# Kernel tuning notes

Hardware: AMD Instinct MI355X
Metric: run time of the kernel (lower is better)

The kernel has to match this reference:

```python
import jax, jax.numpy as jnp
import numpy as np

N, DIN, DOUT, R, H = 3072, 128, 128, 3, 4


def setup_inputs() -> dict:
    key = jax.random.key(0)
    k0, k1, k2, k3 = jax.random.split(key, 4)
    features = jax.random.normal(k0, (N, DIN), jnp.float32)
    adjacency = jax.random.randint(k1, (R, N, N), 0, 2, jnp.int32)
    W = jax.random.normal(k2, (R, DOUT, DIN), jnp.float32) * (1.0 / np.sqrt(DIN))  # Linear weights (out,in)
    hd = DOUT // H
    a = jax.random.normal(k3, (R, 2 * hd), jnp.float32) * (1.0 / np.sqrt(2 * hd))  # attention vectors
    bias = jnp.zeros((DOUT,), jnp.float32)
    return {"features": features, "adjacency": adjacency, "W": W, "a": a,
            "bias": bias, "num_heads": H}


def reference(features, adjacency, W, a, bias, num_heads):
    # features: [N, Din], adjacency: [R, N, N] int, W: [R, Dout, Din],
    # a: [R, 2*head_dim], bias: [Dout]
    Rr, Dout = W.shape[0], W.shape[1]
    Nn = features.shape[0]
    hd = Dout // num_heads
    # per-relation linear transform -> [R, N, H, hd]
    t = jnp.einsum('nd,rod->rno', features, W).reshape(Rr, Nn, num_heads, hd)
    # additive attention: score(i,j,h) = a_src . t[i,h] + a_dst . t[j,h]
    s_src = jnp.einsum('rnhd,rd->rnh', t, a[:, :hd])
    s_dst = jnp.einsum('rnhd,rd->rnh', t, a[:, hd:])
    mask = (adjacency != 0)[..., None]  # [R, N, N, 1]
    # original fills NON-edges with 0 (not -inf), then softmaxes over j incl. zeros
    scores = jnp.where(mask, s_src[:, :, None, :] + s_dst[:, None, :, :], 0.0)  # [R,N,N,H]
    w = jax.nn.softmax(scores, axis=2)
    # aggregation only sums over true edges
    w = jnp.where(mask, w, 0.0)
    out = jnp.einsum('rijh,rjhd->rihd', w, t).reshape(Rr, Nn, Dout)
    return out.mean(axis=0) + bias
```

## Files before the change

kernel.cpp:

```cpp
#include <hip/hip_runtime.h>

typedef float  f32x4  __attribute__((ext_vector_type(4)));
typedef float  f32x2  __attribute__((ext_vector_type(2)));
typedef short  bf16x8 __attribute__((ext_vector_type(8)));
typedef int    i32x4  __attribute__((ext_vector_type(4)));

#define NNODE 3072
#define DIN   128
#define DOUT  128
#define NREL  3
#define NH    4
#define HD    32
#define NC    144
#define KCH   48
#define CHB   9216

static __device__ __forceinline__ unsigned short f2bf(float v) {
  unsigned u = __builtin_bit_cast(unsigned, v);
  u += 0x7FFFu + ((u >> 16) & 1u);
  return (unsigned short)(u >> 16);
}

__global__ __launch_bounds__(256, 1) void k0_init(
    const float* __restrict__ bias, float* __restrict__ out)
{
  const int tid = blockIdx.x * 256 + threadIdx.x;
  f32x4 b = *(const f32x4*)(bias + (tid & 31) * 4);
  *((f32x4*)out + tid) = b;
}

__global__ __launch_bounds__(256, 1) void k1_prep(
    const float* __restrict__ feat, const float* __restrict__ W,
    const float* __restrict__ av, unsigned short* __restrict__ Mt,
    float* __restrict__ Es)
{
  const int jt = blockIdx.x;
  const int r  = blockIdx.y;
  const int t  = threadIdx.x;
  const int jb = jt * 64;

  __shared__ float Wl[128 * 130];
  __shared__ float Fl[64 * 129];
  __shared__ float Tl[64 * 129];
  __shared__ float El[64 * 5];

  const float* Wr = W + r * DOUT * DIN;
  for (int idx = t * 4; idx < DOUT * DIN; idx += 1024) {
    float4 v = *(const float4*)(Wr + idx);
    int o = idx >> 7, k = idx & 127;
    float* d = Wl + o * 130 + k;
    d[0] = v.x; d[1] = v.y; d[2] = v.z; d[3] = v.w;
  }
  for (int idx = t * 4; idx < 64 * DIN; idx += 1024) {
    float4 v = *(const float4*)(feat + (size_t)jb * DIN + idx);
    int n = idx >> 7, k = idx & 127;
    float* d = Fl + n * 129 + k;
    d[0] = v.x; d[1] = v.y; d[2] = v.z; d[3] = v.w;
  }
  __syncthreads();

  {
    const int ng = t & 15, og = t >> 4;
    float acc[4][8] = {};
    for (int k = 0; k < DIN; k += 4) {
      float wv[4][8];
      #pragma unroll
      for (int oo = 0; oo < 8; ++oo) {
        const float* wr2 = Wl + (og * 8 + oo) * 130 + k;
        f32x2 a01 = *(const f32x2*)wr2;
        f32x2 a23 = *(const f32x2*)(wr2 + 2);
        wv[0][oo] = a01[0]; wv[1][oo] = a01[1];
        wv[2][oo] = a23[0]; wv[3][oo] = a23[1];
      }
      #pragma unroll
      for (int nn = 0; nn < 4; ++nn) {
        const float* fr = Fl + (ng * 4 + nn) * 129 + k;
        float f0 = fr[0], f1 = fr[1], f2 = fr[2], f3 = fr[3];
        #pragma unroll
        for (int oo = 0; oo < 8; ++oo) {
          float s = acc[nn][oo];
          s = fmaf(f0, wv[0][oo], s);
          s = fmaf(f1, wv[1][oo], s);
          s = fmaf(f2, wv[2][oo], s);
          s = fmaf(f3, wv[3][oo], s);
          acc[nn][oo] = s;
        }
      }
    }
    #pragma unroll
    for (int nn = 0; nn < 4; ++nn)
      #pragma unroll
      for (int oo = 0; oo < 8; ++oo)
        Tl[(ng * 4 + nn) * 129 + og * 8 + oo] = acc[nn][oo];
  }
  __syncthreads();

  {
    const int n = t & 63, h = t >> 6;
    const float* tr = Tl + n * 129 + h * HD;
    const float* as = av + r * 2 * HD;
    float ss = 0.f, sd = 0.f;
    #pragma unroll
    for (int d = 0; d < HD; ++d) {
      float tvv = tr[d];
      ss = fmaf(tvv, as[d],      ss);
      sd = fmaf(tvv, as[HD + d], sd);
    }
    Es[((size_t)r * NNODE + jb + n) * NH + h] = expf(ss);
    El[n * 5 + h] = expf(sd);
  }
  __syncthreads();

  {
    const int n = t & 63, cb = t >> 6;
    unsigned short* base = Mt + ((size_t)r * KCH + jt) * CHB;
    const int s = n >> 5, k8 = (n >> 3) & 3, elem = n & 7;
    const int lanebase = k8 * 16;
    #pragma unroll
    for (int ci = 0; ci < 36; ++ci) {
      int c = cb * 36 + ci;
      float v;
      if (c < DOUT)            v = Tl[n * 129 + c] * El[n * 5 + (c >> 5)];
      else if (c < DOUT + NH)  v = El[n * 5 + (c - DOUT)];
      else if (c == DOUT + NH) v = 1.0f;
      else                     v = 0.0f;
      int nt = c >> 4;
      base[(nt * 2 + s) * 512 + (lanebase + (c & 15)) * 8 + elem] = f2bf(v);
    }
  }
}

__global__ __launch_bounds__(192, 1) void k2_agg(
    const int* __restrict__ adj, const unsigned short* __restrict__ Mt,
    const float* __restrict__ Es, float* __restrict__ out)
{
  const int it = blockIdx.x;
  const int r  = blockIdx.y;
  const int t  = threadIdx.x;
  const int wv = t >> 6;
  const int l  = t & 63;
  const int l16 = l & 15, l4 = l >> 4;
  const int ib = it * 16;

  __shared__ __align__(16) int Ash[2][1024];
  __shared__ float red[16 * 145];
  __shared__ float coefL[64];

  const size_t adjBase = (size_t)r * NNODE * NNODE + (size_t)ib * NNODE;
  const int r0row = t >> 4,        r0c = (t & 15) ^ (r0row & 7);
  const int r1row = 12 + (t >> 4), r1c = (t & 15) ^ (r1row & 7);

  #define STAGEA(buf, kc) do {                                                    \
    const int* s0_ = adj + adjBase + (size_t)r0row * NNODE + (kc) * 64 + r0c * 4; \
    __builtin_amdgcn_global_load_lds(                                             \
        (const __attribute__((address_space(1))) void*)s0_,                       \
        (__attribute__((address_space(3))) void*)&Ash[buf][wv * 256], 16, 0, 0);  \
    if (t < 64) {                                                                 \
      const int* s1_ = adj + adjBase + (size_t)r1row * NNODE + (kc) * 64 + r1c * 4; \
      __builtin_amdgcn_global_load_lds(                                           \
          (const __attribute__((address_space(1))) void*)s1_,                     \
          (__attribute__((address_space(3))) void*)&Ash[buf][768], 16, 0, 0);     \
    }                                                                             \
  } while (0)

  const unsigned short* mtc = Mt + (size_t)r * KCH * CHB + (size_t)wv * 6 * 512 + (size_t)l * 8;
  bf16x8 Ba[3][2], Bb[3][2];
  #define LOADB(B, kc) do {                                                       \
    const unsigned short* p_ = mtc + (size_t)(kc) * CHB;                          \
    _Pragma("unroll")                                                             \
    for (int i_ = 0; i_ < 3; ++i_) {                                              \
      B[i_][0] = *(const bf16x8*)(p_ + (i_ * 2 + 0) * 512);                       \
      B[i_][1] = *(const bf16x8*)(p_ + (i_ * 2 + 1) * 512);                       \
    }                                                                             \
  } while (0)

  f32x4 acc[3] = {};
  const int arow = l16 * 64, xm = (l & 7) << 2, koff = l4 * 8;

  #define COMPUTE(buf, B) do {                                                    \
    _Pragma("unroll")                                                             \
    for (int s_ = 0; s_ < 2; ++s_) {                                              \
      i32x4 a0 = *(const i32x4*)&Ash[buf][arow + ((s_ * 32 + koff + 0) ^ xm)];    \
      i32x4 a1 = *(const i32x4*)&Ash[buf][arow + ((s_ * 32 + koff + 4) ^ xm)];    \
      bf16x8 af = __builtin_bit_cast(bf16x8, (i32x4){                             \
        (a0[0] | (a0[1] << 16)) * 0x3F80, (a0[2] | (a0[3] << 16)) * 0x3F80,       \
        (a1[0] | (a1[1] << 16)) * 0x3F80, (a1[2] | (a1[3] << 16)) * 0x3F80 });    \
      _Pragma("unroll")                                                           \
      for (int i_ = 0; i_ < 3; ++i_)                                              \
        acc[i_] = __builtin_amdgcn_mfma_f32_16x16x32_bf16(af, B[i_][s_], acc[i_], 0, 0, 0); \
    }                                                                             \
  } while (0)

  STAGEA(0, 0); LOADB(Ba, 0);
  __syncthreads();
  #pragma unroll 1
  for (int kc = 0; kc < KCH; kc += 2) {
    STAGEA(1, kc + 1); LOADB(Bb, kc + 1);
    COMPUTE(0, Ba);
    __syncthreads();
    if (kc + 2 < KCH) { STAGEA(0, kc + 2); LOADB(Ba, kc + 2); }
    COMPUTE(1, Bb);
    __syncthreads();
  }

  #pragma unroll
  for (int i = 0; i < 3; ++i) {
    int nt = wv * 3 + i;
    #pragma unroll
    for (int rg = 0; rg < 4; ++rg)
      red[(l4 * 4 + rg) * 145 + nt * 16 + l16] = acc[i][rg];
  }
  __syncthreads();

  if (t < 64) {
    int row = t >> 2, h = t & 3;
    float es = Es[((size_t)r * NNODE + ib + row) * NH + h];
    float V  = red[row * 145 + DOUT + h];
    float dg = red[row * 145 + DOUT + NH];
    coefL[row * 4 + h] = es / fmaf(es, V, (float)NNODE - dg) * (1.0f / NREL);
  }
  __syncthreads();

  for (int idx = t; idx < 16 * DOUT; idx += 192) {
    int row = idx >> 7, c = idx & 127;
    atomicAdd(&out[(size_t)(ib + row) * DOUT + c],
              coefL[row * 4 + (c >> 5)] * red[row * 145 + c]);
  }
  #undef STAGEA
  #undef LOADB
  #undef COMPUTE
}

extern "C" void kernel_launch(void* const* d_in, const int* in_sizes, int n_in,
                              void* d_out, int out_size, void* d_ws, size_t ws_size,
                              hipStream_t stream) {
  const float* feat = (const float*)d_in[0];
  const int*   adj  = (const int*)d_in[1];
  const float* W    = (const float*)d_in[2];
  const float* av   = (const float*)d_in[3];
  const float* bias = (const float*)d_in[4];

  char* ws = (char*)d_ws;
  unsigned short* Mt = (unsigned short*)ws;
  float* Es = (float*)(ws + 2654208);

  hipLaunchKernelGGL(k0_init, dim3(384), dim3(256), 0, stream, bias, (float*)d_out);
  hipLaunchKernelGGL(k1_prep, dim3(48, 3), dim3(256), 0, stream, feat, W, av, Mt, Es);
  hipLaunchKernelGGL(k2_agg,  dim3(192, 3), dim3(192), 0, stream, adj, Mt, Es, (float*)d_out);
}
```

Before: 63.58 us.

## Use 32-row tiles with 4 waves and triple-buffered adjacency pipeline in aggregation

The aggregation kernel now processes 32 destination rows per block with 256 threads instead of 16 rows with 192, so each wave computes a 2x3 MFMA tile and reuses B fragments across two row groups. The adjacency staging moves from double to triple buffering, using a manual vmcnt wait and a single barrier per chunk instead of two syncthreads. The grid is halved to 96x3 blocks and the launch bounds allow 2 blocks per CU. Waves 0-3 each redundantly load and compute the extra 16-column tile of degree and normalization terms, which trades some duplicated MFMA work and more registers for fewer B loads per row.

```diff
diff --git a/kernel.cpp b/kernel.cpp
--- a/kernel.cpp
+++ b/kernel.cpp
@@ -11,7 +11,6 @@
 #define NREL  3
 #define NH    4
 #define HD    32
-#define NC    144
 #define KCH   48
 #define CHB   9216
 
@@ -130,7 +129,7 @@
   }
 }
 
-__global__ __launch_bounds__(192, 1) void k2_agg(
+__global__ __launch_bounds__(256, 2) void k2_agg(
     const int* __restrict__ adj, const unsigned short* __restrict__ Mt,
     const float* __restrict__ Es, float* __restrict__ out)
 {
@@ -140,88 +139,113 @@
   const int wv = t >> 6;
   const int l  = t & 63;
   const int l16 = l & 15, l4 = l >> 4;
-  const int ib = it * 16;
-
-  __shared__ __align__(16) int Ash[2][1024];
-  __shared__ float red[16 * 145];
-  __shared__ float coefL[64];
+  const int ib = it * 32;
+
+  __shared__ __align__(16) int Ash[3 * 2048];
+  __shared__ float red[32 * 145];
+  __shared__ float coefL[128];
 
   const size_t adjBase = (size_t)r * NNODE * NNODE + (size_t)ib * NNODE;
-  const int r0row = t >> 4,        r0c = (t & 15) ^ (r0row & 7);
-  const int r1row = 12 + (t >> 4), r1c = (t & 15) ^ (r1row & 7);
-
-  #define STAGEA(buf, kc) do {                                                    \
-    const int* s0_ = adj + adjBase + (size_t)r0row * NNODE + (kc) * 64 + r0c * 4; \
+  const int srow = t >> 4;
+  const int schunk = (t & 15) ^ (srow & 7);
+  const int* src0 = adj + adjBase + (size_t)srow * NNODE + schunk * 4;
+  const int* src1 = src0 + 16 * NNODE;
+  const int d0 = wv * 256;
+  const int d1 = wv * 256 + 1024;
+
+  #define STAGEA(bufi, kc) do {                                                   \
     __builtin_amdgcn_global_load_lds(                                             \
-        (const __attribute__((address_space(1))) void*)s0_,                       \
-        (__attribute__((address_space(3))) void*)&Ash[buf][wv * 256], 16, 0, 0);  \
-    if (t < 64) {                                                                 \
-      const int* s1_ = adj + adjBase + (size_t)r1row * NNODE + (kc) * 64 + r1c * 4; \
-      __builtin_amdgcn_global_load_lds(                                           \
-          (const __attribute__((address_space(1))) void*)s1_,                     \
-          (__attribute__((address_space(3))) void*)&Ash[buf][768], 16, 0, 0);     \
-    }                                                                             \
-  } while (0)
-
-  const unsigned short* mtc = Mt + (size_t)r * KCH * CHB + (size_t)wv * 6 * 512 + (size_t)l * 8;
-  bf16x8 Ba[3][2], Bb[3][2];
+        (const __attribute__((address_space(1))) void*)(src0 + (kc) * 64),        \
+        (__attribute__((address_space(3))) void*)&Ash[(bufi) * 2048 + d0], 16, 0, 0); \
+    __builtin_amdgcn_global_load_lds(                                             \
+        (const __attribute__((address_space(1))) void*)(src1 + (kc) * 64),        \
+        (__attribute__((address_space(3))) void*)&Ash[(bufi) * 2048 + d1], 16, 0, 0); \
+  } while (0)
+
+  const unsigned short* mtr = Mt + (size_t)r * KCH * CHB + (size_t)l * 8;
   #define LOADB(B, kc) do {                                                       \
-    const unsigned short* p_ = mtc + (size_t)(kc) * CHB;                          \
-    _Pragma("unroll")                                                             \
-    for (int i_ = 0; i_ < 3; ++i_) {                                              \
-      B[i_][0] = *(const bf16x8*)(p_ + (i_ * 2 + 0) * 512);                       \
-      B[i_][1] = *(const bf16x8*)(p_ + (i_ * 2 + 1) * 512);                       \
-    }                                                                             \
-  } while (0)
-
-  f32x4 acc[3] = {};
-  const int arow = l16 * 64, xm = (l & 7) << 2, koff = l4 * 8;
-
-  #define COMPUTE(buf, B) do {                                                    \
+    const unsigned short* p_ = mtr + (size_t)(kc) * CHB;                          \
+    B[0] = *(const bf16x8*)(p_ + (4 * wv + 0) * 512);                             \
+    B[1] = *(const bf16x8*)(p_ + (4 * wv + 1) * 512);                             \
+    B[2] = *(const bf16x8*)(p_ + (4 * wv + 2) * 512);                             \
+    B[3] = *(const bf16x8*)(p_ + (4 * wv + 3) * 512);                             \
+    B[4] = *(const bf16x8*)(p_ + 16 * 512);                                       \
+    B[5] = *(const bf16x8*)(p_ + 17 * 512);                                       \
+  } while (0)
+
+  f32x4 acc00 = {}, acc01 = {}, acc02 = {}, acc10 = {}, acc11 = {}, acc12 = {};
+  const int xm = (l & 7) << 2;
+  const int arow0 = l16 * 64, arow1 = (16 + l16) * 64;
+
+  #define COMPUTE(bufi, B) do {                                                   \
+    const int* Ab = Ash + (bufi) * 2048;                                          \
     _Pragma("unroll")                                                             \
     for (int s_ = 0; s_ < 2; ++s_) {                                              \
-      i32x4 a0 = *(const i32x4*)&Ash[buf][arow + ((s_ * 32 + koff + 0) ^ xm)];    \
-      i32x4 a1 = *(const i32x4*)&Ash[buf][arow + ((s_ * 32 + koff + 4) ^ xm)];    \
-      bf16x8 af = __builtin_bit_cast(bf16x8, (i32x4){                             \
+      const int ko = s_ * 32 + l4 * 8;                                            \
+      i32x4 a0 = *(const i32x4*)&Ab[arow0 + ((ko + 0) ^ xm)];                     \
+      i32x4 a1 = *(const i32x4*)&Ab[arow0 + ((ko + 4) ^ xm)];                     \
+      i32x4 b0 = *(const i32x4*)&Ab[arow1 + ((ko + 0) ^ xm)];                     \
+      i32x4 b1 = *(const i32x4*)&Ab[arow1 + ((ko + 4) ^ xm)];                     \
+      bf16x8 af0 = __builtin_bit_cast(bf16x8, (i32x4){                            \
         (a0[0] | (a0[1] << 16)) * 0x3F80, (a0[2] | (a0[3] << 16)) * 0x3F80,       \
         (a1[0] | (a1[1] << 16)) * 0x3F80, (a1[2] | (a1[3] << 16)) * 0x3F80 });    \
-      _Pragma("unroll")                                                           \
-      for (int i_ = 0; i_ < 3; ++i_)                                              \
-        acc[i_] = __builtin_amdgcn_mfma_f32_16x16x32_bf16(af, B[i_][s_], acc[i_], 0, 0, 0); \
+      bf16x8 af1 = __builtin_bit_cast(bf16x8, (i32x4){                            \
+        (b0[0] | (b0[1] << 16)) * 0x3F80, (b0[2] | (b0[3] << 16)) * 0x3F80,       \
+        (b1[0] | (b1[1] << 16)) * 0x3F80, (b1[2] | (b1[3] << 16)) * 0x3F80 });    \
+      acc00 = __builtin_amdgcn_mfma_f32_16x16x32_bf16(af0, B[0 + s_], acc00, 0, 0, 0); \
+      acc01 = __builtin_amdgcn_mfma_f32_16x16x32_bf16(af0, B[2 + s_], acc01, 0, 0, 0); \
+      acc02 = __builtin_amdgcn_mfma_f32_16x16x32_bf16(af0, B[4 + s_], acc02, 0, 0, 0); \
+      acc10 = __builtin_amdgcn_mfma_f32_16x16x32_bf16(af1, B[0 + s_], acc10, 0, 0, 0); \
+      acc11 = __builtin_amdgcn_mfma_f32_16x16x32_bf16(af1, B[2 + s_], acc11, 0, 0, 0); \
+      acc12 = __builtin_amdgcn_mfma_f32_16x16x32_bf16(af1, B[4 + s_], acc12, 0, 0, 0); \
     }                                                                             \
   } while (0)
 
-  STAGEA(0, 0); LOADB(Ba, 0);
-  __syncthreads();
+  bf16x8 B0[6], B1[6], B2[6];
+
+  STAGEA(0, 0); LOADB(B0, 0);
+  STAGEA(1, 1); LOADB(B1, 1);
+
+  #define ITER(kc, sbuf, cbuf, BL, BC) do {                                       \
+    asm volatile("s_waitcnt vmcnt(8)" ::: "memory");                              \
+    __builtin_amdgcn_s_barrier();                                                 \
+    __builtin_amdgcn_sched_barrier(0);                                            \
+    const int skc = ((kc) + 2 < KCH) ? (kc) + 2 : KCH - 1;                        \
+    STAGEA(sbuf, skc); LOADB(BL, skc);                                            \
+    COMPUTE(cbuf, BC);                                                            \
+  } while (0)
+
   #pragma unroll 1
-  for (int kc = 0; kc < KCH; kc += 2) {
-    STAGEA(1, kc + 1); LOADB(Bb, kc + 1);
-    COMPUTE(0, Ba);
-    __syncthreads();
-    if (kc + 2 < KCH) { STAGEA(0, kc + 2); LOADB(Ba, kc + 2); }
-    COMPUTE(1, Bb);
-    __syncthreads();
+  for (int kc = 0; kc < KCH; kc += 3) {
+    ITER(kc + 0, 2, 0, B2, B0);
+    ITER(kc + 1, 0, 1, B0, B1);
+    ITER(kc + 2, 1, 2, B1, B2);
   }
 
   #pragma unroll
-  for (int i = 0; i < 3; ++i) {
-    int nt = wv * 3 + i;
-    #pragma unroll
-    for (int rg = 0; rg < 4; ++rg)
-      red[(l4 * 4 + rg) * 145 + nt * 16 + l16] = acc[i][rg];
-  }
-  __syncthreads();
-
-  if (t < 64) {
+  for (int j = 0; j < 4; ++j) {
+    red[(l4 * 4 + j) * 145 + (2 * wv + 0) * 16 + l16]      = acc00[j];
+    red[(l4 * 4 + j) * 145 + (2 * wv + 1) * 16 + l16]      = acc01[j];
+    red[(16 + l4 * 4 + j) * 145 + (2 * wv + 0) * 16 + l16] = acc10[j];
+    red[(16 + l4 * 4 + j) * 145 + (2 * wv + 1) * 16 + l16] = acc11[j];
+    if (wv == 0) {
+      red[(l4 * 4 + j) * 145 + 128 + l16]      = acc02[j];
+      red[(16 + l4 * 4 + j) * 145 + 128 + l16] = acc12[j];
+    }
+  }
+  __syncthreads();
+
+  if (t < 128) {
     int row = t >> 2, h = t & 3;
     float es = Es[((size_t)r * NNODE + ib + row) * NH + h];
     float V  = red[row * 145 + DOUT + h];
     float dg = red[row * 145 + DOUT + NH];
-    coefL[row * 4 + h] = es / fmaf(es, V, (float)NNODE - dg) * (1.0f / NREL);
-  }
-  __syncthreads();
-
-  for (int idx = t; idx < 16 * DOUT; idx += 192) {
+    coefL[t] = es / fmaf(es, V, (float)NNODE - dg) * (1.0f / NREL);
+  }
+  __syncthreads();
+
+  #pragma unroll
+  for (int idx = t; idx < 32 * DOUT; idx += 256) {
     int row = idx >> 7, c = idx & 127;
     atomicAdd(&out[(size_t)(ib + row) * DOUT + c],
               coefL[row * 4 + (c >> 5)] * red[row * 145 + c]);
@@ -229,6 +253,7 @@
   #undef STAGEA
   #undef LOADB
   #undef COMPUTE
+  #undef ITER
 }
 
 extern "C" void kernel_launch(void* const* d_in, const int* in_sizes, int n_in,
@@ -246,5 +271,5 @@
 
   hipLaunchKernelGGL(k0_init, dim3(384), dim3(256), 0, stream, bias, (float*)d_out);
   hipLaunchKernelGGL(k1_prep, dim3(48, 3), dim3(256), 0, stream, feat, W, av, Mt, Es);
-  hipLaunchKernelGGL(k2_agg,  dim3(192, 3), dim3(192), 0, stream, adj, Mt, Es, (float*)d_out);
-}
+  hipLaunchKernelGGL(k2_agg,  dim3(96, 3), dim3(256), 0, stream, adj, Mt, Es, (float*)d_out);
+}
```

Result: slower. 68.68 us (+8.0%).
